# Performance work log

Measured on AMD Instinct MI355X. Metric: run time of the kernel, lower is better.

Reference implementation:

```python
import jax, jax.numpy as jnp
import numpy as np

N = 100000   # node_count
F = 128      # dim_in (also top-k pool size: k = ceil(F/N * N) = F)
E = 625000   # edges


def setup_inputs() -> dict:
    key = jax.random.key(0)
    ks = jax.random.split(key, 20)
    s = 1.0 / np.sqrt(F)

    def g(i, shape, scale=s):
        return jax.random.normal(ks[i], shape, dtype=jnp.float32) * scale

    inp = {
        "x": jax.random.normal(ks[0], (N, F), dtype=jnp.float32),
        "edge_index": jax.random.randint(ks[1], (2, E), 0, N),
        "edge_weight": jax.random.uniform(ks[2], (E,), dtype=jnp.float32),
    }
    for l in (1, 2):
        b = 3 + 6 * (l - 1)
        inp[f"p{l}"] = g(b, (F,))              # TopKPooling projection vector
        inp[f"w_ih{l}"] = g(b + 1, (3 * F, F))  # GRU input weights (r,z,n)
        inp[f"w_hh{l}"] = g(b + 2, (3 * F, F))  # GRU hidden weights
        inp[f"b_ih{l}"] = g(b + 3, (3 * F,))
        inp[f"b_hh{l}"] = g(b + 4, (3 * F,))
        inp[f"h0{l}"] = g(b + 5, (F, F))        # EvolveGCNH initial_weight
    inp["lin1_w"] = g(15, (2, F))
    inp["lin1_b"] = g(16, (2,), 0.1)
    inp["lin2_w"] = g(17, (1, 2), 0.5)
    inp["lin2_b"] = g(18, (1,), 0.1)
    return inp


def _gru_step(x_t, h, w_ih, w_hh, b_ih, b_hh):
    # single GRU timestep, batch = F rows, hidden = F
    gi = x_t @ w_ih.T + b_ih
    gh = h @ w_hh.T + b_hh
    i_r, i_z, i_n = jnp.split(gi, 3, axis=-1)
    h_r, h_z, h_n = jnp.split(gh, 3, axis=-1)
    r = jax.nn.sigmoid(i_r + h_r)
    z = jax.nn.sigmoid(i_z + h_z)
    n = jnp.tanh(i_n + r * h_n)
    return (1.0 - z) * n + z * h


def _gcn_conv_fixed_w(x, W, edge_index, edge_weight):
    # GCN with externally supplied weight: out = D^-1/2 (A+I) D^-1/2 (x W)
    row, col = edge_index[0], edge_index[1]
    loops = jnp.arange(N)
    row = jnp.concatenate([row, loops])
    col = jnp.concatenate([col, loops])
    w = jnp.concatenate([edge_weight, jnp.ones((N,), x.dtype)])
    deg = jax.ops.segment_sum(w, col, num_segments=N)
    dinv = jnp.where(deg > 0, jax.lax.rsqrt(deg), 0.0)
    norm = dinv[row] * w * dinv[col]          # [E+N]
    xw = x @ W                                 # [N, F]
    return jax.ops.segment_sum(norm[:, None] * xw[row], col, num_segments=N)


def _evolve_gcnh(x, edge_index, edge_weight, p, w_ih, w_hh, b_ih, b_hh, h0):
    # TopKPooling: score = x@p / ||p||, keep top F nodes, gate by tanh(score)
    score = x @ p / jnp.linalg.norm(p)
    top_vals, top_idx = jax.lax.top_k(score, F)
    x_tilde = x[top_idx] * jnp.tanh(top_vals)[:, None]   # [F, F]
    # evolve weight via one GRU step (hidden = previous/initial weight)
    W = _gru_step(x_tilde, h0, w_ih, w_hh, b_ih, b_hh)   # [F, F]
    return _gcn_conv_fixed_w(x, W, edge_index, edge_weight)


def reference(x, edge_index, edge_weight,
              p1, w_ih1, w_hh1, b_ih1, b_hh1, h01,
              p2, w_ih2, w_hh2, b_ih2, b_hh2, h02,
              lin1_w, lin1_b, lin2_w, lin2_b):
    h = jax.nn.relu(_evolve_gcnh(x, edge_index, edge_weight, p1, w_ih1, w_hh1, b_ih1, b_hh1, h01))
    h = jax.nn.relu(_evolve_gcnh(h, edge_index, edge_weight, p2, w_ih2, w_hh2, b_ih2, b_hh2, h02))
    # dropout(0.4) is identity in eval mode
    h = h @ lin1_w.T + lin1_b
    h = h @ lin2_w.T + lin2_b
    return h  # [N, 1]
```

## Files before the change

kernel.cpp:

```cpp
#include <hip/hip_runtime.h>
#include <cstdint>
#include <cstddef>


#define FDIM 128

typedef __attribute__((ext_vector_type(8))) short bfrag;
typedef __attribute__((ext_vector_type(4))) float f32x4;
typedef __attribute__((ext_vector_type(2))) float f32x2;

__device__ __forceinline__ float wave_sum(float v) {
#pragma unroll
  for (int m = 32; m >= 1; m >>= 1) v += __shfl_xor(v, m, 64);
  return v;
}

__device__ __forceinline__ float sigmoidf_(float x) {
  return 1.0f / (1.0f + expf(-x));
}

__device__ __forceinline__ unsigned omap(float f) {
  unsigned u = __float_as_uint(f);
  return (u & 0x80000000u) ? ~u : (u | 0x80000000u);
}

__device__ __forceinline__ int xcd_chunk(int b, int nb) {
  return (b & 7) * (nb >> 3) + (b >> 3);
}

__device__ __forceinline__ int swz(int row, int colb) {
  return row * 256 + (colb ^ ((row & 7) << 4));
}


__global__ void k_edge_deg(const int* __restrict__ ei, const float* __restrict__ ew,
                           float* deg, int* cnt, int E) {
  int e = blockIdx.x * blockDim.x + threadIdx.x;
  if (e < E) {
    int c = ei[E + e];
    atomicAdd(&deg[c], ew[e]);
    atomicAdd(&cnt[c], 1);
  }
}

__global__ void k_scan1(const int* __restrict__ cnt, int* bsum,
                        const float* __restrict__ deg, float* __restrict__ dinv, int n) {
  __shared__ int s[256];
  int b = blockIdx.x, t = threadIdx.x;
  int base = b * 1024;
  int v = 0;
#pragma unroll
  for (int j = 0; j < 4; j++) {
    int i = base + j * 256 + t;
    if (i < n) { v += cnt[i]; dinv[i] = 1.0f / sqrtf(1.0f + deg[i]); }
  }
  s[t] = v; __syncthreads();
  for (int off = 128; off > 0; off >>= 1) { if (t < off) s[t] += s[t + off]; __syncthreads(); }
  if (t == 0) bsum[b] = s[0];
}

__global__ __launch_bounds__(128) void k_scan2_setup(
    int* bsum, int nb, int* rstartN,
    const float* p1, const float* p2, float* invn1, float* invn2,
    const float* l1w, const float* l1b, const float* l2w, const float* l2b,
    float* v, float* cc) {
  __shared__ int s[1024];
  int t = threadIdx.x;
  for (int i = t; i < nb; i += 128) s[i] = bsum[i];
  __syncthreads();
  if (t == 0) {
    int run = 0;
    for (int b = 0; b < nb; b++) { int x = s[b]; s[b] = run; run += x; }
    s[1023] = run;
  }
  __syncthreads();
  for (int i = t; i < nb; i += 128) bsum[i] = s[i];
  if (t == 0) rstartN[0] = s[1023];
  int wv = t >> 6, l = t & 63;
  const float* p = wv ? p2 : p1;
  float2 pv = ((const float2*)p)[l];
  float ss = wave_sum(pv.x * pv.x + pv.y * pv.y);
  if (l == 0) (wv ? invn2 : invn1)[0] = 1.0f / sqrtf(ss);
  v[t] = l2w[0] * l1w[t] + l2w[1] * l1w[128 + t];
  if (t == 0) cc[0] = l2w[0] * l1b[0] + l2w[1] * l1b[1] + l2b[0];
}

__global__ __launch_bounds__(1024) void k_scan3(const int* __restrict__ cnt,
                                                const int* __restrict__ bsum,
                                                int* rstart, int* rnext, int n) {
  __shared__ int s[1024];
  int b = blockIdx.x, t = threadIdx.x;
  int i = b * 1024 + t;
  int v = (i < n) ? cnt[i] : 0;
  s[t] = v; __syncthreads();
  for (int off = 1; off < 1024; off <<= 1) {
    int tmp = (t >= off) ? s[t - off] : 0;
    __syncthreads();
    s[t] += tmp;
    __syncthreads();
  }
  if (i < n) { int ex = bsum[b] + s[t] - v; rstart[i] = ex; rnext[i] = ex; }
}

__global__ void k_fill(const int* __restrict__ ei, const float* __restrict__ ew,
                       const float* __restrict__ dinv, int* rnext, int2* pay, int E) {
  int e = blockIdx.x * blockDim.x + threadIdx.x;
  if (e < E) {
    int r = ei[e];
    int c = ei[E + e];
    float nm = dinv[r] * ew[e] * dinv[c];
    int pos = atomicAdd(&rnext[c], 1);
    pay[pos] = make_int2(r, __float_as_int(nm));
  }
}


__global__ void k_sampdots(const float* __restrict__ x, const float* __restrict__ p,
                           const float* __restrict__ invn, float* __restrict__ samp,
                           int stride) {
  int l = threadIdx.x & 63;
  int w = blockIdx.x * 4 + (threadIdx.x >> 6);
  float2 pv = ((const float2*)p)[l];
  float inv = invn[0];
#pragma unroll
  for (int r = 0; r < 4; r++) {
    int si = w * 4 + r;
    float2 a = ((const float2*)(x + (size_t)(si * stride) * FDIM))[l];
    float s = wave_sum(a.x * pv.x + a.y * pv.y) * inv;
    if (l == 0) samp[si] = s;
  }
}

template <int STRIDED>
__global__ __launch_bounds__(256) void k_thr16(const float* __restrict__ src, int stride,
                                               float* __restrict__ thr) {
  __shared__ float a[2048];
  int t = threadIdx.x;
  for (int i = t; i < 2048; i += 256)
    a[i] = STRIDED ? src[(size_t)i * stride] : src[i];
  __syncthreads();
  int g = blockIdx.x * 256 + t;
  int j = g >> 2, sub = g & 3;
  float v = a[j];
  int gt = 0, eq = 0;
  const float4* a4 = (const float4*)(a + sub * 512);
#pragma unroll 8
  for (int i = 0; i < 128; i++) {
    float4 b = a4[i];
    gt += (b.x > v) + (b.y > v) + (b.z > v) + (b.w > v);
    eq += (b.x == v) + (b.y == v) + (b.z == v) + (b.w == v);
  }
  gt += __shfl_xor(gt, 1, 64); eq += __shfl_xor(eq, 1, 64);
  gt += __shfl_xor(gt, 2, 64); eq += __shfl_xor(eq, 2, 64);
  if (sub == 0 && gt <= 15 && gt + eq > 15) thr[0] = v;
}

__global__ void k_scorecollect(const float* __restrict__ x, const float* __restrict__ p,
                               const float* __restrict__ invn, const float* __restrict__ thr,
                               unsigned long long* __restrict__ candk, int* __restrict__ csel,
                               int n) {
  int l = threadIdx.x & 63;
  int eb = xcd_chunk(blockIdx.x, gridDim.x);
  int base = (eb * 4 + (threadIdx.x >> 6)) * 16;
  if (base >= n) return;
  float2 pv = ((const float2*)p)[l];
  float inv = invn[0], th = thr[0];
  int lim = min(16, n - base);
  for (int r = 0; r < lim; r++) {
    float2 a = ((const float2*)(x + (size_t)(base + r) * FDIM))[l];
    float s = wave_sum(a.x * pv.x + a.y * pv.y) * inv;
    if (l == 0 && s >= th) {
      int pos = atomicAdd(csel, 1);
      if (pos < 4096)
        candk[pos] = ((unsigned long long)omap(s) << 32) | (unsigned)(~(unsigned)(base + r));
    }
  }
}

__global__ void k_collect(const float* __restrict__ sc, const float* __restrict__ thr,
                          unsigned long long* candk, int* csel, int n) {
  int i = blockIdx.x * blockDim.x + threadIdx.x;
  if (i >= n) return;
  float s = sc[i];
  if (s >= thr[0]) {
    int pos = atomicAdd(csel, 1);
    if (pos < 4096)
      candk[pos] = ((unsigned long long)omap(s) << 32) | (unsigned)(~(unsigned)i);
  }
}

__global__ __launch_bounds__(1024) void k_sel(const unsigned long long* __restrict__ candk,
                                              const int* __restrict__ csel,
                                              int* tidx, float* ttanh) {
  __shared__ unsigned long long a[4104];
  int t = threadIdx.x;
  int nc = csel[0]; if (nc > 4096) nc = 4096;
  int ncp = (nc + 7) & ~7;
  for (int i = t; i < ncp; i += 1024) a[i] = (i < nc) ? candk[i] : 0ULL;
  __syncthreads();
  for (int j = t; j < nc; j += 1024) {
    unsigned long long key = a[j];
    int r = 0;
#pragma unroll 8
    for (int i = 0; i < ncp; i++) r += (a[i] > key);
    if (r < 128) {
      unsigned idx = ~(unsigned)key;
      unsigned hi = (unsigned)(key >> 32);
      unsigned u = (hi & 0x80000000u) ? (hi ^ 0x80000000u) : ~hi;
      tidx[r] = (int)idx;
      ttanh[r] = tanhf(__uint_as_float(u));
    }
  }
}


__global__ __launch_bounds__(384) void k_gru(const float* __restrict__ xin,
                                             const int* __restrict__ tidx,
                                             const float* __restrict__ ttanh,
                                             const float* __restrict__ wih,
                                             const float* __restrict__ whh,
                                             const float* __restrict__ bih,
                                             const float* __restrict__ bhh,
                                             const float* __restrict__ h0,
                                             unsigned short* __restrict__ WT_hi,
                                             unsigned short* __restrict__ WT_lo) {
  __shared__ float xt[128], hs[128], gis[384], ghs[384];
  int r = blockIdx.x, t = threadIdx.x;
  if (t < 128) {
    int idx = tidx[r];
    xt[t] = xin[(size_t)idx * FDIM + t] * ttanh[r];
    hs[t] = h0[r * FDIM + t];
  }
  __syncthreads();
  float gi = bih[t], gh = bhh[t];
  const float4* wi4 = (const float4*)(wih + (size_t)t * FDIM);
  const float4* wh4 = (const float4*)(whh + (size_t)t * FDIM);
#pragma unroll 8
  for (int k = 0; k < 32; k++) {
    float4 av = wi4[k], bv = wh4[k];
    gi += av.x * xt[4 * k] + av.y * xt[4 * k + 1] + av.z * xt[4 * k + 2] + av.w * xt[4 * k + 3];
    gh += bv.x * hs[4 * k] + bv.y * hs[4 * k + 1] + bv.z * hs[4 * k + 2] + bv.w * hs[4 * k + 3];
  }
  gis[t] = gi; ghs[t] = gh;
  __syncthreads();
  if (t < 128) {
    float rg = sigmoidf_(gis[t] + ghs[t]);
    float zg = sigmoidf_(gis[t + 128] + ghs[t + 128]);
    float ng = tanhf(gis[t + 256] + rg * ghs[t + 256]);
    float w = (1.0f - zg) * ng + zg * hs[t];
    unsigned u = __float_as_uint(w);
    float res = w - __uint_as_float(u & 0xFFFF0000u);
    WT_hi[t * FDIM + r] = (unsigned short)(u >> 16);
    WT_lo[t * FDIM + r] = (unsigned short)(__float_as_uint(res) >> 16);
  }
}


template <int OUTBF16>
__global__ __launch_bounds__(256) void k_gemm4(const float* __restrict__ X,
                                               const unsigned short* __restrict__ BTh,
                                               const unsigned short* __restrict__ BTl,
                                               float* __restrict__ Y,
                                               unsigned short* __restrict__ Y2, int nrows) {
  __shared__ unsigned short sBh[128 * 128];
  __shared__ unsigned short sBl[128 * 128];
  int tid = threadIdx.x;
  int eb = xcd_chunk(blockIdx.x, gridDim.x);
  int rblk = eb * 128;
  if (rblk >= nrows) return;
  for (int i = tid; i < 2048; i += 256) {
    int row = i >> 4, colb = (i & 15) << 4;
    *(uint4*)((char*)sBh + swz(row, colb)) = ((const uint4*)BTh)[i];
    *(uint4*)((char*)sBl + swz(row, colb)) = ((const uint4*)BTl)[i];
  }
  __syncthreads();
  int wv = tid >> 6, l = tid & 63;
  int lcol = l & 15;
  int kgrp = (l >> 4) * 8;

  for (int tile = 0; tile < 2; tile++) {
    int r0 = rblk + wv * 32 + tile * 16;
    if (r0 >= nrows) break;
    int arow = min(r0 + lcol, nrows - 1);
    f32x4 acc[8];
#pragma unroll
    for (int c = 0; c < 8; c++) acc[c] = (f32x4){0.f, 0.f, 0.f, 0.f};
    const float* xp = X + (size_t)arow * FDIM + kgrp;
#pragma unroll
    for (int ks = 0; ks < 4; ks++) {
      float4 v0 = *(const float4*)(xp + ks * 32);
      float4 v1 = *(const float4*)(xp + ks * 32 + 4);
      float xs[8] = {v0.x, v0.y, v0.z, v0.w, v1.x, v1.y, v1.z, v1.w};
      bfrag ah, al;
#pragma unroll
      for (int i = 0; i < 8; i++) {
        unsigned u = __float_as_uint(xs[i]);
        float res = xs[i] - __uint_as_float(u & 0xFFFF0000u);
        ah[i] = (short)(u >> 16);
        al[i] = (short)(__float_as_uint(res) >> 16);
      }
      int colb = (ks * 32 + kgrp) * 2;
#pragma unroll
      for (int ct = 0; ct < 8; ct++) {
        int off = swz(ct * 16 + lcol, colb);
        bfrag bh = *(const bfrag*)((const char*)sBh + off);
        bfrag bl = *(const bfrag*)((const char*)sBl + off);
        acc[ct] = __builtin_amdgcn_mfma_f32_16x16x32_bf16(ah, bh, acc[ct], 0, 0, 0);
        acc[ct] = __builtin_amdgcn_mfma_f32_16x16x32_bf16(ah, bl, acc[ct], 0, 0, 0);
        acc[ct] = __builtin_amdgcn_mfma_f32_16x16x32_bf16(al, bh, acc[ct], 0, 0, 0);
      }
    }
    int rbase = r0 + (l >> 4) * 4;
#pragma unroll
    for (int ct = 0; ct < 8; ct++) {
      int col = ct * 16 + lcol;
#pragma unroll
      for (int r = 0; r < 4; r++) {
        int row = rbase + r;
        if (row < nrows) {
          if (OUTBF16) {
            unsigned u = __float_as_uint(acc[ct][r]);
            Y2[(size_t)row * FDIM + col] = (unsigned short)((u + 0x8000u) >> 16);
          } else {
            Y[(size_t)row * FDIM + col] = acc[ct][r];
          }
        }
      }
    }
  }
}


template <int FUSE>
__global__ void k_gather(const void* __restrict__ xwv, const float* __restrict__ dinv,
                         const int* __restrict__ rstart,
                         const int2* __restrict__ pay, float* __restrict__ outH,
                         float* __restrict__ outF,
                         const float* __restrict__ p2, const float* __restrict__ invn2,
                         float* __restrict__ sc,
                         const float* __restrict__ vvec, const float* __restrict__ cc,
                         int n) {
  int wv = threadIdx.x >> 6, l = threadIdx.x & 63;
  int eb = xcd_chunk(blockIdx.x, gridDim.x);
  int c = eb * 4 + wv;
  if (c >= n) return;
  float dc = dinv[c];
  float ax, ay;
  unsigned long long xwb;
  if (FUSE == 0) {
    const float* xw = (const float*)xwv;
    float2 v = ((const float2*)(xw + (size_t)c * FDIM))[l];
    ax = dc * dc * v.x; ay = dc * dc * v.y;
    xwb = (unsigned long long)(const char*)xwv + ((size_t)l << 3);
  } else {
    const unsigned short* xw2 = (const unsigned short*)xwv;
    unsigned u = *(const unsigned*)(xw2 + (size_t)c * FDIM + l * 2);
    ax = dc * dc * __uint_as_float(u << 16);
    ay = dc * dc * __uint_as_float(u & 0xFFFF0000u);
    xwb = (unsigned long long)(const char*)xwv + ((size_t)l << 2);
  }
  int st = rstart[c], cn = rstart[c + 1] - st;
  for (int q0 = 0; q0 < cn; q0 += 64) {
    int2 ep = (q0 + l < cn) ? pay[st + q0 + l] : make_int2(c, 0);
    int m = min(64, cn - q0);
    for (int g = 0; g < m; g += 8) {
      unsigned long long addr[8];
      float w[8];
#pragma unroll
      for (int u = 0; u < 8; u++) {
        int r = __shfl(ep.x, g + u, 64);
        w[u] = __int_as_float(__shfl(ep.y, g + u, 64));
        addr[u] = xwb + ((unsigned long long)(unsigned)r << (FUSE ? 8 : 9));
      }
      if (FUSE == 0) {
        f32x2 ev[8];
#pragma unroll
        for (int u = 0; u < 8; u++)
          asm volatile("global_load_dwordx2 %0, %1, off" : "=v"(ev[u]) : "v"(addr[u]));
        asm volatile("s_waitcnt vmcnt(0)" ::: "memory");
        __builtin_amdgcn_sched_barrier(0);
#pragma unroll
        for (int u = 0; u < 8; u++) { ax += w[u] * ev[u][0]; ay += w[u] * ev[u][1]; }
      } else {
        unsigned uv[8];
#pragma unroll
        for (int u = 0; u < 8; u++)
          asm volatile("global_load_dword %0, %1, off" : "=v"(uv[u]) : "v"(addr[u]));
        asm volatile("s_waitcnt vmcnt(0)" ::: "memory");
        __builtin_amdgcn_sched_barrier(0);
#pragma unroll
        for (int u = 0; u < 8; u++) {
          ax += w[u] * __uint_as_float(uv[u] << 16);
          ay += w[u] * __uint_as_float(uv[u] & 0xFFFF0000u);
        }
      }
    }
  }
  float r0 = fmaxf(ax, 0.0f), r1 = fmaxf(ay, 0.0f);
  if (FUSE == 0) {
    ((float2*)(outH + (size_t)c * FDIM))[l] = make_float2(r0, r1);
    float2 pv = ((const float2*)p2)[l];
    float s = wave_sum(r0 * pv.x + r1 * pv.y);
    if (l == 0) sc[c] = s * invn2[0];
  } else {
    float2 vv = ((const float2*)vvec)[l];
    float s = wave_sum(r0 * vv.x + r1 * vv.y);
    if (l == 0) outF[c] = s + cc[0];
  }
}


extern "C" void kernel_launch(void* const* d_in, const int* in_sizes, int n_in,
                              void* d_out, int out_size, void* d_ws, size_t ws_size,
                              hipStream_t stream) {
  const float* x    = (const float*)d_in[0];
  const int*   ei   = (const int*)d_in[1];
  const float* ew   = (const float*)d_in[2];
  const float* p1   = (const float*)d_in[3];
  const float* wih1 = (const float*)d_in[4];
  const float* whh1 = (const float*)d_in[5];
  const float* bih1 = (const float*)d_in[6];
  const float* bhh1 = (const float*)d_in[7];
  const float* h01  = (const float*)d_in[8];
  const float* p2   = (const float*)d_in[9];
  const float* wih2 = (const float*)d_in[10];
  const float* whh2 = (const float*)d_in[11];
  const float* bih2 = (const float*)d_in[12];
  const float* bhh2 = (const float*)d_in[13];
  const float* h02  = (const float*)d_in[14];
  const float* l1w  = (const float*)d_in[15];
  const float* l1b  = (const float*)d_in[16];
  const float* l2w  = (const float*)d_in[17];
  const float* l2b  = (const float*)d_in[18];
  float* out = (float*)d_out;

  const int N = in_sizes[0] / FDIM;
  const int E = in_sizes[2];

  size_t off = 0;
  auto alloc = [&](size_t bytes) -> char* {
    char* p = (char*)d_ws + off;
    off = (off + bytes + 255) & ~(size_t)255;
    return p;
  };
  float* deg   = (float*)alloc((size_t)N * 4);
  int*   cnt   = (int*)alloc((size_t)N * 4);
  int*   csel1 = (int*)alloc(8);
  int*   csel2 = (int*)alloc(8);
  size_t zero_span = (size_t)((char*)(csel2 + 2) - (char*)deg);
  float* scores = (float*)alloc((size_t)N * 4);
  unsigned long long* candk = (unsigned long long*)alloc(4096 * 8);
  int*   tidx  = (int*)alloc(128 * 4);
  float* ttanh = (float*)alloc(128 * 4);
  float* invn1 = (float*)alloc(4);
  float* invn2 = (float*)alloc(4);
  float* thr1  = (float*)alloc(4);
  float* thr2  = (float*)alloc(4);
  float* samp  = (float*)alloc(2048 * 4);
  float* dinv  = (float*)alloc((size_t)N * 4);
  int*   rstart= (int*)alloc((size_t)(N + 1) * 4);
  int*   rnext = (int*)alloc((size_t)N * 4);
  const int nb = (N + 1023) / 1024;
  int*   bsum  = (int*)alloc((size_t)nb * 4);
  int2*  pay   = (int2*)alloc((size_t)E * 8);
  float* vvec  = (float*)alloc(128 * 4);
  float* cc    = (float*)alloc(4);
  unsigned short* WTh = (unsigned short*)alloc(128 * 128 * 2);
  unsigned short* WTl = (unsigned short*)alloc(128 * 128 * 2);
  float* xw    = (float*)alloc((size_t)N * FDIM * 4);
  unsigned short* xw2 = (unsigned short*)alloc((size_t)N * FDIM * 2);
  float* h1    = (float*)alloc((size_t)N * FDIM * 4);
  (void)ws_size; (void)n_in; (void)out_size;

  const int scoreblocks  = (((N + 15) / 16 + 3) / 4 + 7) & ~7;
  const int gemmblocks   = ((N + 127) / 128 + 7) & ~7;
  const int gatherblocks = (N + 3) / 4;
  const int sampstride   = N / 2048;

  hipMemsetAsync(deg, 0, zero_span, stream);
  k_edge_deg<<<(E + 255) / 256, 256, 0, stream>>>(ei, ew, deg, cnt, E);
  k_scan1<<<nb, 256, 0, stream>>>(cnt, bsum, deg, dinv, N);
  k_scan2_setup<<<1, 128, 0, stream>>>(bsum, nb, rstart + N, p1, p2, invn1, invn2,
                                       l1w, l1b, l2w, l2b, vvec, cc);
  k_scan3<<<nb, 1024, 0, stream>>>(cnt, bsum, rstart, rnext, N);
  k_fill<<<(E + 255) / 256, 256, 0, stream>>>(ei, ew, dinv, rnext, pay, E);

  k_sampdots<<<128, 256, 0, stream>>>(x, p1, invn1, samp, sampstride);
  k_thr16<0><<<32, 256, 0, stream>>>(samp, 1, thr1);
  k_scorecollect<<<scoreblocks, 256, 0, stream>>>(x, p1, invn1, thr1, candk, csel1, N);
  k_sel<<<1, 1024, 0, stream>>>(candk, csel1, tidx, ttanh);
  k_gru<<<128, 384, 0, stream>>>(x, tidx, ttanh, wih1, whh1, bih1, bhh1, h01, WTh, WTl);
  k_gemm4<0><<<gemmblocks, 256, 0, stream>>>(x, WTh, WTl, xw, nullptr, N);
  k_gather<0><<<gatherblocks, 256, 0, stream>>>(xw, dinv, rstart, pay, h1, nullptr,
                                                p2, invn2, scores, nullptr, nullptr, N);

  k_thr16<1><<<32, 256, 0, stream>>>(scores, sampstride, thr2);
  k_collect<<<(N + 255) / 256, 256, 0, stream>>>(scores, thr2, candk, csel2, N);
  k_sel<<<1, 1024, 0, stream>>>(candk, csel2, tidx, ttanh);
  k_gru<<<128, 384, 0, stream>>>(h1, tidx, ttanh, wih2, whh2, bih2, bhh2, h02, WTh, WTl);
  k_gemm4<1><<<gemmblocks, 256, 0, stream>>>(h1, WTh, WTl, nullptr, xw2, N);
  k_gather<1><<<gatherblocks, 256, 0, stream>>>(xw2, dinv, rstart, pay, nullptr, out,
                                                nullptr, nullptr, nullptr, vvec, cc, N);
}
```

Measured before the change: 345.6 us.

## Reorder GCN as aggregate-then-transform and fuse scoring into gather and GEMM

Uses associativity, A(XW) = (AX)W, so the sparse aggregation runs on raw x before the dense GEMM, and the layer-1 top-k scoring moves into the first gather pass. That removes the separate score-collect kernel. The layer-1 GEMM now applies ReLU, writes bf16 h1 and computes the layer-2 scores. Layer 2 aggregates bf16 h1 first, and its GEMM fuses ReLU with the final linear projection, so the fp32 xw intermediates and one read of x disappear. The cost is that h1 is stored in bf16 and the layer-2 GEMM drops the low-part correction on A, which slightly reduces accuracy.

```diff
diff --git a/kernel.cpp b/kernel.cpp
--- a/kernel.cpp
+++ b/kernel.cpp
@@ -155,28 +155,6 @@
   if (sub == 0 && gt <= 15 && gt + eq > 15) thr[0] = v;
 }
 
-__global__ void k_scorecollect(const float* __restrict__ x, const float* __restrict__ p,
-                               const float* __restrict__ invn, const float* __restrict__ thr,
-                               unsigned long long* __restrict__ candk, int* __restrict__ csel,
-                               int n) {
-  int l = threadIdx.x & 63;
-  int eb = xcd_chunk(blockIdx.x, gridDim.x);
-  int base = (eb * 4 + (threadIdx.x >> 6)) * 16;
-  if (base >= n) return;
-  float2 pv = ((const float2*)p)[l];
-  float inv = invn[0], th = thr[0];
-  int lim = min(16, n - base);
-  for (int r = 0; r < lim; r++) {
-    float2 a = ((const float2*)(x + (size_t)(base + r) * FDIM))[l];
-    float s = wave_sum(a.x * pv.x + a.y * pv.y) * inv;
-    if (l == 0 && s >= th) {
-      int pos = atomicAdd(csel, 1);
-      if (pos < 4096)
-        candk[pos] = ((unsigned long long)omap(s) << 32) | (unsigned)(~(unsigned)(base + r));
-    }
-  }
-}
-
 __global__ void k_collect(const float* __restrict__ sc, const float* __restrict__ thr,
                           unsigned long long* candk, int* csel, int n) {
   int i = blockIdx.x * blockDim.x + threadIdx.x;
@@ -214,7 +192,8 @@
 }
 
 
-__global__ __launch_bounds__(384) void k_gru(const float* __restrict__ xin,
+template <int BF16IN>
+__global__ __launch_bounds__(384) void k_gru(const void* __restrict__ xinv,
                                              const int* __restrict__ tidx,
                                              const float* __restrict__ ttanh,
                                              const float* __restrict__ wih,
@@ -228,7 +207,14 @@
   int r = blockIdx.x, t = threadIdx.x;
   if (t < 128) {
     int idx = tidx[r];
-    xt[t] = xin[(size_t)idx * FDIM + t] * ttanh[r];
+    float xv;
+    if (BF16IN) {
+      unsigned short u = ((const unsigned short*)xinv)[(size_t)idx * FDIM + t];
+      xv = __uint_as_float((unsigned)u << 16);
+    } else {
+      xv = ((const float*)xinv)[(size_t)idx * FDIM + t];
+    }
+    xt[t] = xv * ttanh[r];
     hs[t] = h0[r * FDIM + t];
   }
   __syncthreads();
@@ -256,12 +242,17 @@
 }
 
 
-template <int OUTBF16>
-__global__ __launch_bounds__(256) void k_gemm4(const float* __restrict__ X,
+template <int MODE>
+__global__ __launch_bounds__(256) void k_gemm5(const float* __restrict__ Af,
+                                               const unsigned short* __restrict__ Ab,
                                                const unsigned short* __restrict__ BTh,
                                                const unsigned short* __restrict__ BTl,
-                                               float* __restrict__ Y,
-                                               unsigned short* __restrict__ Y2, int nrows) {
+                                               unsigned short* __restrict__ Y2,
+                                               float* __restrict__ scOut,
+                                               const float* __restrict__ pvec,
+                                               const float* __restrict__ invn2,
+                                               const float* __restrict__ cc,
+                                               int nrows) {
   __shared__ unsigned short sBh[128 * 128];
   __shared__ unsigned short sBl[128 * 128];
   int tid = threadIdx.x;
@@ -278,6 +269,11 @@
   int lcol = l & 15;
   int kgrp = (l >> 4) * 8;
 
+  float pv[8];
+#pragma unroll
+  for (int ct = 0; ct < 8; ct++) pv[ct] = pvec[ct * 16 + lcol];
+  float scale = (MODE == 1) ? invn2[0] : cc[0];
+
   for (int tile = 0; tile < 2; tile++) {
     int r0 = rblk + wv * 32 + tile * 16;
     if (r0 >= nrows) break;
@@ -285,19 +281,23 @@
     f32x4 acc[8];
 #pragma unroll
     for (int c = 0; c < 8; c++) acc[c] = (f32x4){0.f, 0.f, 0.f, 0.f};
-    const float* xp = X + (size_t)arow * FDIM + kgrp;
 #pragma unroll
     for (int ks = 0; ks < 4; ks++) {
-      float4 v0 = *(const float4*)(xp + ks * 32);
-      float4 v1 = *(const float4*)(xp + ks * 32 + 4);
-      float xs[8] = {v0.x, v0.y, v0.z, v0.w, v1.x, v1.y, v1.z, v1.w};
       bfrag ah, al;
-#pragma unroll
-      for (int i = 0; i < 8; i++) {
-        unsigned u = __float_as_uint(xs[i]);
-        float res = xs[i] - __uint_as_float(u & 0xFFFF0000u);
-        ah[i] = (short)(u >> 16);
-        al[i] = (short)(__float_as_uint(res) >> 16);
+      if (MODE == 1) {
+        const float* xp = Af + (size_t)arow * FDIM + kgrp + ks * 32;
+        float4 v0 = *(const float4*)(xp);
+        float4 v1 = *(const float4*)(xp + 4);
+        float xs[8] = {v0.x, v0.y, v0.z, v0.w, v1.x, v1.y, v1.z, v1.w};
+#pragma unroll
+        for (int i = 0; i < 8; i++) {
+          unsigned u = __float_as_uint(xs[i]);
+          float res = xs[i] - __uint_as_float(u & 0xFFFF0000u);
+          ah[i] = (short)(u >> 16);
+          al[i] = (short)(__float_as_uint(res) >> 16);
+        }
+      } else {
+        ah = *(const bfrag*)(Ab + (size_t)arow * FDIM + kgrp + ks * 32);
       }
       int colb = (ks * 32 + kgrp) * 2;
 #pragma unroll
@@ -307,23 +307,38 @@
         bfrag bl = *(const bfrag*)((const char*)sBl + off);
         acc[ct] = __builtin_amdgcn_mfma_f32_16x16x32_bf16(ah, bh, acc[ct], 0, 0, 0);
         acc[ct] = __builtin_amdgcn_mfma_f32_16x16x32_bf16(ah, bl, acc[ct], 0, 0, 0);
-        acc[ct] = __builtin_amdgcn_mfma_f32_16x16x32_bf16(al, bh, acc[ct], 0, 0, 0);
+        if (MODE == 1)
+          acc[ct] = __builtin_amdgcn_mfma_f32_16x16x32_bf16(al, bh, acc[ct], 0, 0, 0);
       }
     }
     int rbase = r0 + (l >> 4) * 4;
+    float part[4] = {0.f, 0.f, 0.f, 0.f};
 #pragma unroll
     for (int ct = 0; ct < 8; ct++) {
       int col = ct * 16 + lcol;
+#pragma unroll
+      for (int r = 0; r < 4; r++) {
+        int row = rbase + r;
+        float rl = fmaxf(acc[ct][r], 0.0f);
+        part[r] += rl * pv[ct];
+        if (MODE == 1 && row < nrows) {
+          unsigned u = __float_as_uint(rl);
+          Y2[(size_t)row * FDIM + col] = (unsigned short)((u + 0x8000u) >> 16);
+        }
+      }
+    }
+#pragma unroll
+    for (int r = 0; r < 4; r++) {
+#pragma unroll
+      for (int m = 1; m < 16; m <<= 1) part[r] += __shfl_xor(part[r], m, 64);
+    }
+    if (lcol == 0) {
 #pragma unroll
       for (int r = 0; r < 4; r++) {
         int row = rbase + r;
         if (row < nrows) {
-          if (OUTBF16) {
-            unsigned u = __float_as_uint(acc[ct][r]);
-            Y2[(size_t)row * FDIM + col] = (unsigned short)((u + 0x8000u) >> 16);
-          } else {
-            Y[(size_t)row * FDIM + col] = acc[ct][r];
-          }
+          if (MODE == 1) scOut[row] = part[r] * scale;
+          else           scOut[row] = part[r] + scale;
         }
       }
     }
@@ -331,33 +346,35 @@
 }
 
 
-template <int FUSE>
-__global__ void k_gather(const void* __restrict__ xwv, const float* __restrict__ dinv,
-                         const int* __restrict__ rstart,
-                         const int2* __restrict__ pay, float* __restrict__ outH,
-                         float* __restrict__ outF,
-                         const float* __restrict__ p2, const float* __restrict__ invn2,
-                         float* __restrict__ sc,
-                         const float* __restrict__ vvec, const float* __restrict__ cc,
-                         int n) {
+template <int L>
+__global__ void k_gather5(const void* __restrict__ inv, void* __restrict__ outv,
+                          const float* __restrict__ dinv,
+                          const int* __restrict__ rstart,
+                          const int2* __restrict__ pay,
+                          const float* __restrict__ p1, const float* __restrict__ invn1,
+                          const float* __restrict__ thr1,
+                          unsigned long long* __restrict__ candk, int* __restrict__ csel,
+                          int n) {
   int wv = threadIdx.x >> 6, l = threadIdx.x & 63;
   int eb = xcd_chunk(blockIdx.x, gridDim.x);
   int c = eb * 4 + wv;
   if (c >= n) return;
   float dc = dinv[c];
-  float ax, ay;
-  unsigned long long xwb;
-  if (FUSE == 0) {
-    const float* xw = (const float*)xwv;
-    float2 v = ((const float2*)(xw + (size_t)c * FDIM))[l];
+  float ax, ay, sx0, sx1;
+  unsigned long long base;
+  if (L == 1) {
+    const float* in = (const float*)inv;
+    float2 v = ((const float2*)(in + (size_t)c * FDIM))[l];
+    sx0 = v.x; sx1 = v.y;
     ax = dc * dc * v.x; ay = dc * dc * v.y;
-    xwb = (unsigned long long)(const char*)xwv + ((size_t)l << 3);
+    base = (unsigned long long)(const char*)inv + ((size_t)l << 3);
   } else {
-    const unsigned short* xw2 = (const unsigned short*)xwv;
-    unsigned u = *(const unsigned*)(xw2 + (size_t)c * FDIM + l * 2);
+    const unsigned short* in = (const unsigned short*)inv;
+    unsigned u = *(const unsigned*)(in + (size_t)c * FDIM + l * 2);
+    sx0 = sx1 = 0.f;
     ax = dc * dc * __uint_as_float(u << 16);
     ay = dc * dc * __uint_as_float(u & 0xFFFF0000u);
-    xwb = (unsigned long long)(const char*)xwv + ((size_t)l << 2);
+    base = (unsigned long long)(const char*)inv + ((size_t)l << 2);
   }
   int st = rstart[c], cn = rstart[c + 1] - st;
   for (int q0 = 0; q0 < cn; q0 += 64) {
@@ -370,9 +387,9 @@
       for (int u = 0; u < 8; u++) {
         int r = __shfl(ep.x, g + u, 64);
         w[u] = __int_as_float(__shfl(ep.y, g + u, 64));
-        addr[u] = xwb + ((unsigned long long)(unsigned)r << (FUSE ? 8 : 9));
+        addr[u] = base + ((unsigned long long)(unsigned)r << (L == 1 ? 9 : 8));
       }
-      if (FUSE == 0) {
+      if (L == 1) {
         f32x2 ev[8];
 #pragma unroll
         for (int u = 0; u < 8; u++)
@@ -396,16 +413,21 @@
       }
     }
   }
-  float r0 = fmaxf(ax, 0.0f), r1 = fmaxf(ay, 0.0f);
-  if (FUSE == 0) {
-    ((float2*)(outH + (size_t)c * FDIM))[l] = make_float2(r0, r1);
-    float2 pv = ((const float2*)p2)[l];
-    float s = wave_sum(r0 * pv.x + r1 * pv.y);
-    if (l == 0) sc[c] = s * invn2[0];
+  if (L == 1) {
+    float* out = (float*)outv;
+    ((float2*)(out + (size_t)c * FDIM))[l] = make_float2(ax, ay);
+    float2 pvv = ((const float2*)p1)[l];
+    float s = wave_sum(sx0 * pvv.x + sx1 * pvv.y) * invn1[0];
+    if (l == 0 && s >= thr1[0]) {
+      int pos = atomicAdd(csel, 1);
+      if (pos < 4096)
+        candk[pos] = ((unsigned long long)omap(s) << 32) | (unsigned)(~(unsigned)c);
+    }
   } else {
-    float2 vv = ((const float2*)vvec)[l];
-    float s = wave_sum(r0 * vv.x + r1 * vv.y);
-    if (l == 0) outF[c] = s + cc[0];
+    unsigned* out = (unsigned*)outv;
+    unsigned lo = (__float_as_uint(ax) + 0x8000u) >> 16;
+    unsigned hi = (__float_as_uint(ay) + 0x8000u) >> 16;
+    out[(size_t)c * (FDIM / 2) + l] = lo | (hi << 16);
   }
 }
 
@@ -448,7 +470,7 @@
   int*   csel1 = (int*)alloc(8);
   int*   csel2 = (int*)alloc(8);
   size_t zero_span = (size_t)((char*)(csel2 + 2) - (char*)deg);
-  float* scores = (float*)alloc((size_t)N * 4);
+  float* sc2   = (float*)alloc((size_t)N * 4);
   unsigned long long* candk = (unsigned long long*)alloc(4096 * 8);
   int*   tidx  = (int*)alloc(128 * 4);
   float* ttanh = (float*)alloc(128 * 4);
@@ -467,12 +489,11 @@
   float* cc    = (float*)alloc(4);
   unsigned short* WTh = (unsigned short*)alloc(128 * 128 * 2);
   unsigned short* WTl = (unsigned short*)alloc(128 * 128 * 2);
-  float* xw    = (float*)alloc((size_t)N * FDIM * 4);
-  unsigned short* xw2 = (unsigned short*)alloc((size_t)N * FDIM * 2);
-  float* h1    = (float*)alloc((size_t)N * FDIM * 4);
+  float* g1    = (float*)alloc((size_t)N * FDIM * 4);
+  unsigned short* h1 = (unsigned short*)alloc((size_t)N * FDIM * 2);
+  unsigned short* g2 = (unsigned short*)alloc((size_t)N * FDIM * 2);
   (void)ws_size; (void)n_in; (void)out_size;
 
-  const int scoreblocks  = (((N + 15) / 16 + 3) / 4 + 7) & ~7;
   const int gemmblocks   = ((N + 127) / 128 + 7) & ~7;
   const int gatherblocks = (N + 3) / 4;
   const int sampstride   = N / 2048;
@@ -487,18 +508,19 @@
 
   k_sampdots<<<128, 256, 0, stream>>>(x, p1, invn1, samp, sampstride);
   k_thr16<0><<<32, 256, 0, stream>>>(samp, 1, thr1);
-  k_scorecollect<<<scoreblocks, 256, 0, stream>>>(x, p1, invn1, thr1, candk, csel1, N);
+  k_gather5<1><<<gatherblocks, 256, 0, stream>>>(x, g1, dinv, rstart, pay,
+                                                 p1, invn1, thr1, candk, csel1, N);
   k_sel<<<1, 1024, 0, stream>>>(candk, csel1, tidx, ttanh);
-  k_gru<<<128, 384, 0, stream>>>(x, tidx, ttanh, wih1, whh1, bih1, bhh1, h01, WTh, WTl);
-  k_gemm4<0><<<gemmblocks, 256, 0, stream>>>(x, WTh, WTl, xw, nullptr, N);
-  k_gather<0><<<gatherblocks, 256, 0, stream>>>(xw, dinv, rstart, pay, h1, nullptr,
-                                                p2, invn2, scores, nullptr, nullptr, N);
-
-  k_thr16<1><<<32, 256, 0, stream>>>(scores, sampstride, thr2);
-  k_collect<<<(N + 255) / 256, 256, 0, stream>>>(scores, thr2, candk, csel2, N);
+  k_gru<0><<<128, 384, 0, stream>>>(x, tidx, ttanh, wih1, whh1, bih1, bhh1, h01, WTh, WTl);
+  k_gemm5<1><<<gemmblocks, 256, 0, stream>>>(g1, nullptr, WTh, WTl, h1, sc2,
+                                             p2, invn2, cc, N);
+
+  k_thr16<1><<<32, 256, 0, stream>>>(sc2, sampstride, thr2);
+  k_collect<<<(N + 255) / 256, 256, 0, stream>>>(sc2, thr2, candk, csel2, N);
   k_sel<<<1, 1024, 0, stream>>>(candk, csel2, tidx, ttanh);
-  k_gru<<<128, 384, 0, stream>>>(h1, tidx, ttanh, wih2, whh2, bih2, bhh2, h02, WTh, WTl);
-  k_gemm4<1><<<gemmblocks, 256, 0, stream>>>(h1, WTh, WTl, nullptr, xw2, N);
-  k_gather<1><<<gatherblocks, 256, 0, stream>>>(xw2, dinv, rstart, pay, nullptr, out,
-                                                nullptr, nullptr, nullptr, vvec, cc, N);
-}
+  k_gru<1><<<128, 384, 0, stream>>>(h1, tidx, ttanh, wih2, whh2, bih2, bhh2, h02, WTh, WTl);
+  k_gather5<2><<<gatherblocks, 256, 0, stream>>>(h1, g2, dinv, rstart, pay,
+                                                 nullptr, nullptr, nullptr, nullptr, nullptr, N);
+  k_gemm5<2><<<gemmblocks, 256, 0, stream>>>(nullptr, g2, WTh, WTl, nullptr, out,
+                                             vvec, nullptr, cc, N);
+}
```

Result: faster. 323.0 us (-6.5%).
